# Optimization experiments

Measured on AMD Instinct MI355X. Metric: run time of the kernel, lower is better.

Reference implementation:

```python
import jax, jax.numpy as jnp
import numpy as np

NUM_HEADS = 8
DIM_HEAD = 48
SCALE = DIM_HEAD ** -0.5


def setup_inputs() -> dict:
    key = jax.random.key(0)
    k1, k2, k3 = jax.random.split(key, 3)
    B, N, D = 4, 2048, 384
    inner = NUM_HEADS * DIM_HEAD  # 384
    x = jax.random.normal(k1, (B, N, D), dtype=jnp.float32)
    # store weights in [in, out] layout (equivalent to torch Linear W.T)
    Wqkv = jax.random.normal(k2, (D, 3 * inner), dtype=jnp.float32) * (D ** -0.5)
    Wproj = jax.random.normal(k3, (inner, D), dtype=jnp.float32) * (inner ** -0.5)
    bproj = jnp.zeros((D,), dtype=jnp.float32)
    return {"x": x, "Wqkv": Wqkv, "Wproj": Wproj, "bproj": bproj}


def reference(x, Wqkv, Wproj, bproj):
    B, N, D = x.shape
    h, dh = NUM_HEADS, DIM_HEAD
    C = h * dh
    # fused QKV projection (qkv_bias=False)
    qkv = (x @ Wqkv).reshape(B, N, 3, h, dh)
    q = qkv[:, :, 0].transpose(0, 2, 1, 3)  # [B, h, N, dh]
    k = qkv[:, :, 1].transpose(0, 2, 1, 3)
    v = qkv[:, :, 2].transpose(0, 2, 1, 3)
    # naive attention: materialize [B, h, N, N] scores
    sim = jnp.einsum("bhqd,bhkd->bhqk", q, k) * SCALE
    attn = jax.nn.softmax(sim, axis=-1)
    out = jnp.einsum("bhqk,bhkd->bhqd", attn, v)  # [B, h, N, dh]
    out = out.transpose(0, 2, 1, 3).reshape(B, N, C)
    return out @ Wproj + bproj
```

## Files before the change

### kernel.cpp

```cpp
#include <hip/hip_runtime.h>
#include <hip/hip_bf16.h>


typedef _Float16 f16x8 __attribute__((ext_vector_type(8)));
typedef _Float16 f16x4 __attribute__((ext_vector_type(4)));
typedef float    f32x4 __attribute__((ext_vector_type(4)));
typedef float    f32x16 __attribute__((ext_vector_type(16)));

#define QSCL 0.20822035963448658f

__global__ __launch_bounds__(256) void prep(const float* __restrict__ wq,
                                            const float* __restrict__ wp,
                                            _Float16* __restrict__ wqt,
                                            _Float16* __restrict__ wpt)
{
    __shared__ _Float16 t[64][65];
    const int blk = blockIdx.x, tid = threadIdx.x;
    const float* src; _Float16* dst; int Nn, k0, n0;
    if (blk < 108) {
        src = wq; dst = wqt; Nn = 1152;
        k0 = (blk % 6) * 64; n0 = (blk / 6) * 64;
    } else {
        const int b2 = blk - 108;
        src = wp; dst = wpt; Nn = 384;
        k0 = (b2 % 6) * 64; n0 = (b2 / 6) * 64;
    }
    #pragma unroll
    for (int i = 0; i < 16; i++) {
        const int id = tid + i * 256;
        const int k = id >> 6, n = id & 63;
        t[k][n] = (_Float16)src[(size_t)(k0 + k) * Nn + n0 + n];
    }
    __syncthreads();
    #pragma unroll
    for (int i = 0; i < 16; i++) {
        const int id = tid + i * 256;
        const int n = id >> 6, k = id & 63;
        dst[(size_t)(n0 + n) * 384 + k0 + k] = t[k][n];
    }
}

union QkvSmem {
    struct { _Float16 As[128][72]; _Float16 Bs[64][72]; } g;
    _Float16 Ts[64][136];
    _Float16 Ts2[128][72];
};

__global__ __launch_bounds__(256) void qkv_f16(const float* __restrict__ X,
                                               const _Float16* __restrict__ Bt,
                                               _Float16* __restrict__ qh,
                                               _Float16* __restrict__ kh,
                                               _Float16* __restrict__ vt)
{
    __shared__ QkvSmem sm;
    const int tid = threadIdx.x;
    const int w = tid >> 6, lane = tid & 63, cl = lane & 15, quad = lane >> 4;
    const int bm = blockIdx.x, bn = blockIdx.y;

    f32x4 acc[2][4];
    const f32x4 z4 = {0.f, 0.f, 0.f, 0.f};
    #pragma unroll
    for (int mi = 0; mi < 2; mi++)
        #pragma unroll
        for (int t = 0; t < 4; t++) acc[mi][t] = z4;

    const int ar = tid >> 3, ac = (tid & 7) * 8;
    const float*    Ag = X  + (size_t)(bm * 128 + ar) * 384 + ac;
    const _Float16* Bg = Bt + (size_t)(bn * 64  + ar) * 384 + ac;

    float4 pa0[4], pa1[4];
    f16x8 pb[2];
    #pragma unroll
    for (int j = 0; j < 4; j++) {
        pa0[j] = *(const float4*)(Ag + (size_t)(32 * j) * 384);
        pa1[j] = *(const float4*)(Ag + (size_t)(32 * j) * 384 + 4);
    }
    #pragma unroll
    for (int j = 0; j < 2; j++) pb[j] = *(const f16x8*)(Bg + (size_t)(32 * j) * 384);

    for (int k0 = 0; k0 < 384; k0 += 64) {
        __syncthreads();
        #pragma unroll
        for (int j = 0; j < 4; j++) {
            f16x8 hh;
            hh[0] = (_Float16)pa0[j].x; hh[1] = (_Float16)pa0[j].y;
            hh[2] = (_Float16)pa0[j].z; hh[3] = (_Float16)pa0[j].w;
            hh[4] = (_Float16)pa1[j].x; hh[5] = (_Float16)pa1[j].y;
            hh[6] = (_Float16)pa1[j].z; hh[7] = (_Float16)pa1[j].w;
            *(f16x8*)&sm.g.As[ar + 32 * j][ac] = hh;
        }
        #pragma unroll
        for (int j = 0; j < 2; j++) *(f16x8*)&sm.g.Bs[ar + 32 * j][ac] = pb[j];
        __syncthreads();
        if (k0 + 64 < 384) {
            #pragma unroll
            for (int j = 0; j < 4; j++) {
                pa0[j] = *(const float4*)(Ag + (size_t)(32 * j) * 384 + k0 + 64);
                pa1[j] = *(const float4*)(Ag + (size_t)(32 * j) * 384 + k0 + 68);
            }
            #pragma unroll
            for (int j = 0; j < 2; j++)
                pb[j] = *(const f16x8*)(Bg + (size_t)(32 * j) * 384 + k0 + 64);
        }
        #pragma unroll
        for (int kh2 = 0; kh2 < 2; kh2++) {
            f16x8 bf[4];
            #pragma unroll
            for (int t = 0; t < 4; t++)
                bf[t] = *(const f16x8*)&sm.g.Bs[t * 16 + cl][kh2 * 32 + quad * 8];
            #pragma unroll
            for (int mi = 0; mi < 2; mi++) {
                const f16x8 af = *(const f16x8*)&sm.g.As[w * 32 + mi * 16 + cl][kh2 * 32 + quad * 8];
                #pragma unroll
                for (int t = 0; t < 4; t++)
                    acc[mi][t] = __builtin_amdgcn_mfma_f32_16x16x32_f16(af, bf[t], acc[mi][t], 0, 0, 0);
            }
        }
    }

    const int s = (bn * 64) / 384;
    if (s == 2) {
        __syncthreads();
        #pragma unroll
        for (int t = 0; t < 4; t++)
            #pragma unroll
            for (int mi = 0; mi < 2; mi++)
                #pragma unroll
                for (int r = 0; r < 4; r++)
                    sm.Ts[t * 16 + cl][w * 32 + mi * 16 + quad * 4 + r] =
                        (_Float16)acc[mi][t][r];
        __syncthreads();
        const int colbase = bn * 64 - 768;
        const int b  = (bm * 128) >> 11;
        const int n0 = (bm * 128) & 2047;
        #pragma unroll
        for (int i = 0; i < 4; i++) {
            const int c = i * 256 + tid;
            const int col = c >> 4, nc = c & 15;
            const int gcol = colbase + col;
            const int head = gcol / 48, d = gcol - head * 48;
            const int bh = b * 8 + head;
            *(f16x8*)&vt[(size_t)(bh * 48 + d) * 2048 + n0 + nc * 8] =
                *(const f16x8*)&sm.Ts[col][nc * 8];
        }
    } else {
        __syncthreads();
        const float scl = (s == 0) ? QSCL : 1.0f;
        #pragma unroll
        for (int t = 0; t < 4; t++)
            #pragma unroll
            for (int mi = 0; mi < 2; mi++)
                #pragma unroll
                for (int r = 0; r < 4; r++)
                    sm.Ts2[w * 32 + mi * 16 + quad * 4 + r][t * 16 + cl] =
                        (_Float16)(acc[mi][t][r] * scl);
        __syncthreads();
        _Float16* dst = (s == 0) ? qh : kh;
        const int colbase = bn * 64 - s * 384;
        const int b  = (bm * 128) >> 11;
        const int n0 = (bm * 128) & 2047;
        #pragma unroll
        for (int i = 0; i < 4; i++) {
            const int c = i * 256 + tid;
            const int row = c >> 3, ch = c & 7;
            const int gcol = colbase + ch * 8;
            const int head = gcol / 48, d = gcol - head * 48;
            const int bh = b * 8 + head;
            *(f16x8*)&dst[(size_t)(bh * 2048 + n0 + row) * 48 + d] =
                *(const f16x8*)&sm.Ts2[row][ch * 8];
        }
    }
}

union AttnSmem {
    struct {
        _Float16 Ks[64][56];
        _Float16 Vts[64][72];
    } a;
    _Float16 Ot[128][58];
};

__global__ __launch_bounds__(256) void attn_f16(const _Float16* __restrict__ qh,
                                                const _Float16* __restrict__ kh,
                                                const _Float16* __restrict__ vt,
                                                _Float16* __restrict__ ab)
{
    __shared__ AttnSmem sm;
    const int tid = threadIdx.x;
    const int w = tid >> 6, lane = tid & 63, ln = lane & 31, h = lane >> 5;
    const int bh = blockIdx.x, qt = blockIdx.y;

    for (int i = tid; i < 16 * 72; i += 256) {
        const int r = 48 + i / 72, c = i - (i / 72) * 72;
        sm.a.Vts[r][c] = (r == 48) ? (_Float16)1.0f : (_Float16)0.0f;
    }

    f16x8 qf[3];
    {
        const _Float16* qp = qh + (size_t)(bh * 2048 + qt * 128 + w * 32 + ln) * 48 + 8 * h;
        qf[0] = *(const f16x8*)qp;
        qf[1] = *(const f16x8*)(qp + 16);
        qf[2] = *(const f16x8*)(qp + 32);
    }

    f32x16 o0, o1;
    #pragma unroll
    for (int r = 0; r < 16; r++) { o0[r] = 0.f; o1[r] = 0.f; }

    const _Float16* kbase = kh + (size_t)bh * 2048 * 48;
    const _Float16* vbase = vt + (size_t)bh * 48 * 2048;

    const int kr0 = tid / 6,         kc0 = (tid % 6) * 8;
    const int kid1 = tid + 256;
    const int kr1 = kid1 / 6,        kc1 = (kid1 % 6) * 8;
    const int vr0 = tid >> 3,        vc0 = (tid & 7) * 8;
    const int vr1 = (tid + 256) >> 3;
    const int vslot_lo = 16 * ((tid & 7) >> 1) + 4 * (tid & 1);
    const _Float16* ks0 = kbase + (size_t)kr0 * 48 + kc0;
    const _Float16* ks1 = kbase + (size_t)kr1 * 48 + kc1;
    const _Float16* vs0 = vbase + (size_t)vr0 * 2048 + vc0;
    const _Float16* vs1 = vbase + (size_t)vr1 * 2048 + vc0;

    f16x8 rk0 = *(const f16x8*)ks0;
    f16x8 rv0 = *(const f16x8*)vs0;
    f16x8 rk1, rv1;
    if (tid < 128) { rk1 = *(const f16x8*)ks1; rv1 = *(const f16x8*)vs1; }

    for (int kt = 0; kt < 2048; kt += 64) {
        __syncthreads();
        *(f16x8*)&sm.a.Ks[kr0][kc0] = rk0;
        {
            const f16x4* rvh = (const f16x4*)&rv0;
            *(f16x4*)&sm.a.Vts[vr0][vslot_lo]     = rvh[0];
            *(f16x4*)&sm.a.Vts[vr0][vslot_lo + 8] = rvh[1];
        }
        if (tid < 128) {
            *(f16x8*)&sm.a.Ks[kr1][kc1] = rk1;
            const f16x4* rvh = (const f16x4*)&rv1;
            *(f16x4*)&sm.a.Vts[vr1][vslot_lo]     = rvh[0];
            *(f16x4*)&sm.a.Vts[vr1][vslot_lo + 8] = rvh[1];
        }
        __syncthreads();
        if (kt + 64 < 2048) {
            rk0 = *(const f16x8*)(ks0 + (size_t)(kt + 64) * 48);
            rv0 = *(const f16x8*)(vs0 + kt + 64);
            if (tid < 128) {
                rk1 = *(const f16x8*)(ks1 + (size_t)(kt + 64) * 48);
                rv1 = *(const f16x8*)(vs1 + kt + 64);
            }
        }

        f32x16 s0, s1;
        #pragma unroll
        for (int r = 0; r < 16; r++) { s0[r] = 0.f; s1[r] = 0.f; }
        #pragma unroll
        for (int i = 0; i < 3; i++) {
            const f16x8 ka0 = *(const f16x8*)&sm.a.Ks[ln][16 * i + 8 * h];
            s0 = __builtin_amdgcn_mfma_f32_32x32x16_f16(ka0, qf[i], s0, 0, 0, 0);
            const f16x8 ka1 = *(const f16x8*)&sm.a.Ks[32 + ln][16 * i + 8 * h];
            s1 = __builtin_amdgcn_mfma_f32_32x32x16_f16(ka1, qf[i], s1, 0, 0, 0);
        }

        f16x8 pbf[4];
        #pragma unroll
        for (int j = 0; j < 8; j++) {
            pbf[0][j] = (_Float16)exp2f(s0[j]);
            pbf[1][j] = (_Float16)exp2f(s0[8 + j]);
            pbf[2][j] = (_Float16)exp2f(s1[j]);
            pbf[3][j] = (_Float16)exp2f(s1[8 + j]);
        }

        #pragma unroll
        for (int c = 0; c < 4; c++) {
            const f16x8 av0 = *(const f16x8*)&sm.a.Vts[ln][16 * c + 8 * h];
            o0 = __builtin_amdgcn_mfma_f32_32x32x16_f16(av0, pbf[c], o0, 0, 0, 0);
            const f16x8 av1 = *(const f16x8*)&sm.a.Vts[32 + ln][16 * c + 8 * h];
            o1 = __builtin_amdgcn_mfma_f32_32x32x16_f16(av1, pbf[c], o1, 0, 0, 0);
        }
    }

    const float lr  = __shfl(o1[8], ln);
    const float inv = 1.f / lr;

    __syncthreads();
    #pragma unroll
    for (int r = 0; r < 16; r++)
        sm.Ot[w * 32 + ln][(r & 3) + 8 * (r >> 2) + 4 * h] = (_Float16)(o0[r] * inv);
    #pragma unroll
    for (int r = 0; r < 8; r++)
        sm.Ot[w * 32 + ln][32 + (r & 3) + 8 * (r >> 2) + 4 * h] = (_Float16)(o1[r] * inv);
    __syncthreads();
    const int b = bh >> 3, hd = bh & 7;
    #pragma unroll
    for (int i = 0; i < 3; i++) {
        const int c2 = i * 256 + tid;
        const int row = c2 / 6, ch = c2 % 6;
        const int q = qt * 128 + row;
        *(f16x8*)&ab[(size_t)(b * 2048 + q) * 384 + hd * 48 + ch * 8] =
            *(const f16x8*)&sm.Ot[row][ch * 8];
    }
}

__global__ __launch_bounds__(256) void proj_f16(const _Float16* __restrict__ A,
                                                const _Float16* __restrict__ Bt,
                                                const float* __restrict__ bias,
                                                float* __restrict__ out)
{
    __shared__ _Float16 As[64][72];
    __shared__ _Float16 Bs[64][72];
    const int tid = threadIdx.x;
    const int w = tid >> 6, lane = tid & 63, cl = lane & 15, quad = lane >> 4;
    const int bm = blockIdx.x, bn = blockIdx.y;

    f32x4 acc[4];
    const f32x4 z4 = {0.f, 0.f, 0.f, 0.f};
    #pragma unroll
    for (int t = 0; t < 4; t++) acc[t] = z4;

    const int ar = tid >> 3, ac = (tid & 7) * 8;
    const _Float16* Ag = A  + (size_t)(bm * 64 + ar) * 384 + ac;
    const _Float16* Bg = Bt + (size_t)(bn * 64 + ar) * 384 + ac;

    f16x8 pa[2], pb[2];
    #pragma unroll
    for (int j = 0; j < 2; j++) {
        pa[j] = *(const f16x8*)(Ag + (size_t)(32 * j) * 384);
        pb[j] = *(const f16x8*)(Bg + (size_t)(32 * j) * 384);
    }

    for (int k0 = 0; k0 < 384; k0 += 64) {
        __syncthreads();
        #pragma unroll
        for (int j = 0; j < 2; j++) {
            *(f16x8*)&As[ar + 32 * j][ac] = pa[j];
            *(f16x8*)&Bs[ar + 32 * j][ac] = pb[j];
        }
        __syncthreads();
        if (k0 + 64 < 384) {
            #pragma unroll
            for (int j = 0; j < 2; j++) {
                pa[j] = *(const f16x8*)(Ag + (size_t)(32 * j) * 384 + k0 + 64);
                pb[j] = *(const f16x8*)(Bg + (size_t)(32 * j) * 384 + k0 + 64);
            }
        }
        #pragma unroll
        for (int kh2 = 0; kh2 < 2; kh2++) {
            const f16x8 af = *(const f16x8*)&As[w * 16 + cl][kh2 * 32 + quad * 8];
            #pragma unroll
            for (int t = 0; t < 4; t++) {
                const f16x8 bf = *(const f16x8*)&Bs[t * 16 + cl][kh2 * 32 + quad * 8];
                acc[t] = __builtin_amdgcn_mfma_f32_16x16x32_f16(af, bf, acc[t], 0, 0, 0);
            }
        }
    }

    #pragma unroll
    for (int t = 0; t < 4; t++) {
        const int col = bn * 64 + t * 16 + cl;
        const float bv = bias[col];
        #pragma unroll
        for (int r = 0; r < 4; r++) {
            const int row = bm * 64 + w * 16 + quad * 4 + r;
            out[(size_t)row * 384 + col] = acc[t][r] + bv;
        }
    }
}

extern "C" void kernel_launch(void* const* d_in, const int* in_sizes, int n_in,
                              void* d_out, int out_size, void* d_ws, size_t ws_size,
                              hipStream_t stream) {
    const float* x     = (const float*)d_in[0];
    const float* Wqkv  = (const float*)d_in[1];
    const float* Wproj = (const float*)d_in[2];
    const float* bproj = (const float*)d_in[3];
    float* out = (float*)d_out;

    char* ws = (char*)d_ws;
    _Float16* wqkvt  = (_Float16*)(ws + 0);
    _Float16* wprojt = (_Float16*)(ws + 884736);
    _Float16* qh     = (_Float16*)(ws + 1179648);
    _Float16* kh     = (_Float16*)(ws + 7471104);
    _Float16* vt     = (_Float16*)(ws + 13762560);
    _Float16* ab     = (_Float16*)(ws + 20054016);

    prep<<<144, 256, 0, stream>>>(Wqkv, Wproj, wqkvt, wprojt);
    qkv_f16<<<dim3(64, 18), 256, 0, stream>>>(x, wqkvt, qh, kh, vt);
    attn_f16<<<dim3(32, 16), 256, 0, stream>>>(qh, kh, vt, ab);
    proj_f16<<<dim3(128, 6), 256, 0, stream>>>(ab, wprojt, bproj, out);
}
```

Baseline: 149.5 us.

## Pre-convert X to fp16 in prep and widen QKV GEMM tile to 128x128

The prep kernel gains extra blocks that convert the fp32 input X to fp16 in workspace. The QKV GEMM then loads fp16 A directly and uses a 128x128 output tile with a 32-wide K step instead of 128x64 with 64-wide K. This removes the per-block fp32-to-fp16 conversion that was repeated across all 18 column tiles and halves the grid's A re-reads. In exchange it adds a full write and read of an fp16 copy of X, doubles the accumulator register count, and runs more, shallower K iterations with a sync each.

```diff
diff --git a/kernel.cpp b/kernel.cpp
--- a/kernel.cpp
+++ b/kernel.cpp
@@ -9,44 +9,59 @@
 
 #define QSCL 0.20822035963448658f
 
-__global__ __launch_bounds__(256) void prep(const float* __restrict__ wq,
+__global__ __launch_bounds__(256) void prep(const float4* __restrict__ x,
+                                            const float* __restrict__ wq,
                                             const float* __restrict__ wp,
+                                            f16x4* __restrict__ xh4,
                                             _Float16* __restrict__ wqt,
                                             _Float16* __restrict__ wpt)
 {
     __shared__ _Float16 t[64][65];
     const int blk = blockIdx.x, tid = threadIdx.x;
-    const float* src; _Float16* dst; int Nn, k0, n0;
-    if (blk < 108) {
-        src = wq; dst = wqt; Nn = 1152;
-        k0 = (blk % 6) * 64; n0 = (blk / 6) * 64;
+    if (blk < 144) {
+        const float* src; _Float16* dst; int Nn, k0, n0;
+        if (blk < 108) {
+            src = wq; dst = wqt; Nn = 1152;
+            k0 = (blk % 6) * 64; n0 = (blk / 6) * 64;
+        } else {
+            const int b2 = blk - 108;
+            src = wp; dst = wpt; Nn = 384;
+            k0 = (b2 % 6) * 64; n0 = (b2 / 6) * 64;
+        }
+        #pragma unroll
+        for (int i = 0; i < 16; i++) {
+            const int id = tid + i * 256;
+            const int k = id >> 6, n = id & 63;
+            t[k][n] = (_Float16)src[(size_t)(k0 + k) * Nn + n0 + n];
+        }
+        __syncthreads();
+        #pragma unroll
+        for (int i = 0; i < 16; i++) {
+            const int id = tid + i * 256;
+            const int n = id >> 6, k = id & 63;
+            dst[(size_t)(n0 + n) * 384 + k0 + k] = t[k][n];
+        }
     } else {
-        const int b2 = blk - 108;
-        src = wp; dst = wpt; Nn = 384;
-        k0 = (b2 % 6) * 64; n0 = (b2 / 6) * 64;
-    }
-    #pragma unroll
-    for (int i = 0; i < 16; i++) {
-        const int id = tid + i * 256;
-        const int k = id >> 6, n = id & 63;
-        t[k][n] = (_Float16)src[(size_t)(k0 + k) * Nn + n0 + n];
-    }
-    __syncthreads();
-    #pragma unroll
-    for (int i = 0; i < 16; i++) {
-        const int id = tid + i * 256;
-        const int n = id >> 6, k = id & 63;
-        dst[(size_t)(n0 + n) * 384 + k0 + k] = t[k][n];
+        const int base = (blk - 144) * 3072;
+        #pragma unroll
+        for (int r = 0; r < 12; r++) {
+            const int j = base + r * 256 + tid;
+            const float4 tt = x[j];
+            f16x4 hh;
+            hh[0] = (_Float16)tt.x; hh[1] = (_Float16)tt.y;
+            hh[2] = (_Float16)tt.z; hh[3] = (_Float16)tt.w;
+            xh4[j] = hh;
+        }
     }
 }
 
 union QkvSmem {
-    struct { _Float16 As[128][72]; _Float16 Bs[64][72]; } g;
-    _Float16 Ts[64][136];
-    _Float16 Ts2[128][72];
+    struct { _Float16 As[128][40]; _Float16 Bs[128][40]; } g;
+    _Float16 Ts[128][136];
+    _Float16 Ts2[128][136];
 };
 
-__global__ __launch_bounds__(256) void qkv_f16(const float* __restrict__ X,
+__global__ __launch_bounds__(256) void qkv_f16(const _Float16* __restrict__ A,
                                                const _Float16* __restrict__ Bt,
                                                _Float16* __restrict__ qh,
                                                _Float16* __restrict__ kh,
@@ -57,72 +72,59 @@
     const int w = tid >> 6, lane = tid & 63, cl = lane & 15, quad = lane >> 4;
     const int bm = blockIdx.x, bn = blockIdx.y;
 
-    f32x4 acc[2][4];
+    f32x4 acc[2][8];
     const f32x4 z4 = {0.f, 0.f, 0.f, 0.f};
     #pragma unroll
     for (int mi = 0; mi < 2; mi++)
         #pragma unroll
-        for (int t = 0; t < 4; t++) acc[mi][t] = z4;
-
-    const int ar = tid >> 3, ac = (tid & 7) * 8;
-    const float*    Ag = X  + (size_t)(bm * 128 + ar) * 384 + ac;
-    const _Float16* Bg = Bt + (size_t)(bn * 64  + ar) * 384 + ac;
-
-    float4 pa0[4], pa1[4];
-    f16x8 pb[2];
-    #pragma unroll
-    for (int j = 0; j < 4; j++) {
-        pa0[j] = *(const float4*)(Ag + (size_t)(32 * j) * 384);
-        pa1[j] = *(const float4*)(Ag + (size_t)(32 * j) * 384 + 4);
-    }
-    #pragma unroll
-    for (int j = 0; j < 2; j++) pb[j] = *(const f16x8*)(Bg + (size_t)(32 * j) * 384);
-
-    for (int k0 = 0; k0 < 384; k0 += 64) {
-        __syncthreads();
-        #pragma unroll
-        for (int j = 0; j < 4; j++) {
-            f16x8 hh;
-            hh[0] = (_Float16)pa0[j].x; hh[1] = (_Float16)pa0[j].y;
-            hh[2] = (_Float16)pa0[j].z; hh[3] = (_Float16)pa0[j].w;
-            hh[4] = (_Float16)pa1[j].x; hh[5] = (_Float16)pa1[j].y;
-            hh[6] = (_Float16)pa1[j].z; hh[7] = (_Float16)pa1[j].w;
-            *(f16x8*)&sm.g.As[ar + 32 * j][ac] = hh;
-        }
-        #pragma unroll
-        for (int j = 0; j < 2; j++) *(f16x8*)&sm.g.Bs[ar + 32 * j][ac] = pb[j];
-        __syncthreads();
-        if (k0 + 64 < 384) {
-            #pragma unroll
-            for (int j = 0; j < 4; j++) {
-                pa0[j] = *(const float4*)(Ag + (size_t)(32 * j) * 384 + k0 + 64);
-                pa1[j] = *(const float4*)(Ag + (size_t)(32 * j) * 384 + k0 + 68);
+        for (int t = 0; t < 8; t++) acc[mi][t] = z4;
+
+    const int ar = tid >> 2, ac = (tid & 3) * 8;
+    const _Float16* Ag = A  + (size_t)(bm * 128 + ar) * 384 + ac;
+    const _Float16* Bg = Bt + (size_t)(bn * 128 + ar) * 384 + ac;
+
+    f16x8 pa[2], pb[2];
+    #pragma unroll
+    for (int j = 0; j < 2; j++) {
+        pa[j] = *(const f16x8*)(Ag + (size_t)(64 * j) * 384);
+        pb[j] = *(const f16x8*)(Bg + (size_t)(64 * j) * 384);
+    }
+
+    for (int k0 = 0; k0 < 384; k0 += 32) {
+        __syncthreads();
+        #pragma unroll
+        for (int j = 0; j < 2; j++) {
+            *(f16x8*)&sm.g.As[ar + 64 * j][ac] = pa[j];
+            *(f16x8*)&sm.g.Bs[ar + 64 * j][ac] = pb[j];
+        }
+        __syncthreads();
+        if (k0 + 32 < 384) {
+            #pragma unroll
+            for (int j = 0; j < 2; j++) {
+                pa[j] = *(const f16x8*)(Ag + (size_t)(64 * j) * 384 + k0 + 32);
+                pb[j] = *(const f16x8*)(Bg + (size_t)(64 * j) * 384 + k0 + 32);
             }
-            #pragma unroll
-            for (int j = 0; j < 2; j++)
-                pb[j] = *(const f16x8*)(Bg + (size_t)(32 * j) * 384 + k0 + 64);
-        }
-        #pragma unroll
-        for (int kh2 = 0; kh2 < 2; kh2++) {
-            f16x8 bf[4];
-            #pragma unroll
-            for (int t = 0; t < 4; t++)
-                bf[t] = *(const f16x8*)&sm.g.Bs[t * 16 + cl][kh2 * 32 + quad * 8];
-            #pragma unroll
-            for (int mi = 0; mi < 2; mi++) {
-                const f16x8 af = *(const f16x8*)&sm.g.As[w * 32 + mi * 16 + cl][kh2 * 32 + quad * 8];
-                #pragma unroll
-                for (int t = 0; t < 4; t++)
-                    acc[mi][t] = __builtin_amdgcn_mfma_f32_16x16x32_f16(af, bf[t], acc[mi][t], 0, 0, 0);
-            }
-        }
-    }
-
-    const int s = (bn * 64) / 384;
+        }
+        f16x8 bf[8];
+        #pragma unroll
+        for (int t = 0; t < 8; t++)
+            bf[t] = *(const f16x8*)&sm.g.Bs[t * 16 + cl][quad * 8];
+        #pragma unroll
+        for (int mi = 0; mi < 2; mi++) {
+            const f16x8 af = *(const f16x8*)&sm.g.As[w * 32 + mi * 16 + cl][quad * 8];
+            #pragma unroll
+            for (int t = 0; t < 8; t++)
+                acc[mi][t] = __builtin_amdgcn_mfma_f32_16x16x32_f16(af, bf[t], acc[mi][t], 0, 0, 0);
+        }
+    }
+
+    const int s = (bn * 128) / 384;
+    const int b  = (bm * 128) >> 11;
+    const int n0 = (bm * 128) & 2047;
     if (s == 2) {
         __syncthreads();
         #pragma unroll
-        for (int t = 0; t < 4; t++)
+        for (int t = 0; t < 8; t++)
             #pragma unroll
             for (int mi = 0; mi < 2; mi++)
                 #pragma unroll
@@ -130,11 +132,9 @@
                     sm.Ts[t * 16 + cl][w * 32 + mi * 16 + quad * 4 + r] =
                         (_Float16)acc[mi][t][r];
         __syncthreads();
-        const int colbase = bn * 64 - 768;
-        const int b  = (bm * 128) >> 11;
-        const int n0 = (bm * 128) & 2047;
-        #pragma unroll
-        for (int i = 0; i < 4; i++) {
+        const int colbase = bn * 128 - 768;
+        #pragma unroll
+        for (int i = 0; i < 8; i++) {
             const int c = i * 256 + tid;
             const int col = c >> 4, nc = c & 15;
             const int gcol = colbase + col;
@@ -147,7 +147,7 @@
         __syncthreads();
         const float scl = (s == 0) ? QSCL : 1.0f;
         #pragma unroll
-        for (int t = 0; t < 4; t++)
+        for (int t = 0; t < 8; t++)
             #pragma unroll
             for (int mi = 0; mi < 2; mi++)
                 #pragma unroll
@@ -156,13 +156,11 @@
                         (_Float16)(acc[mi][t][r] * scl);
         __syncthreads();
         _Float16* dst = (s == 0) ? qh : kh;
-        const int colbase = bn * 64 - s * 384;
-        const int b  = (bm * 128) >> 11;
-        const int n0 = (bm * 128) & 2047;
-        #pragma unroll
-        for (int i = 0; i < 4; i++) {
+        const int colbase = bn * 128 - s * 384;
+        #pragma unroll
+        for (int i = 0; i < 8; i++) {
             const int c = i * 256 + tid;
-            const int row = c >> 3, ch = c & 7;
+            const int row = c >> 4, ch = c & 15;
             const int gcol = colbase + ch * 8;
             const int head = gcol / 48, d = gcol - head * 48;
             const int bh = b * 8 + head;
@@ -376,15 +374,17 @@
     float* out = (float*)d_out;
 
     char* ws = (char*)d_ws;
-    _Float16* wqkvt  = (_Float16*)(ws + 0);
-    _Float16* wprojt = (_Float16*)(ws + 884736);
-    _Float16* qh     = (_Float16*)(ws + 1179648);
-    _Float16* kh     = (_Float16*)(ws + 7471104);
-    _Float16* vt     = (_Float16*)(ws + 13762560);
-    _Float16* ab     = (_Float16*)(ws + 20054016);
-
-    prep<<<144, 256, 0, stream>>>(Wqkv, Wproj, wqkvt, wprojt);
-    qkv_f16<<<dim3(64, 18), 256, 0, stream>>>(x, wqkvt, qh, kh, vt);
+    _Float16* xh     = (_Float16*)(ws + 0);
+    _Float16* wqkvt  = (_Float16*)(ws + 6291456);
+    _Float16* wprojt = (_Float16*)(ws + 7176192);
+    _Float16* qh     = (_Float16*)(ws + 7471104);
+    _Float16* kh     = (_Float16*)(ws + 13762560);
+    _Float16* vt     = (_Float16*)(ws + 20054016);
+    _Float16* ab     = (_Float16*)(ws + 26345472);
+
+    prep<<<400, 256, 0, stream>>>((const float4*)x, Wqkv, Wproj,
+                                  (f16x4*)xh, wqkvt, wprojt);
+    qkv_f16<<<dim3(64, 9), 256, 0, stream>>>(xh, wqkvt, qh, kh, vt);
     attn_f16<<<dim3(32, 16), 256, 0, stream>>>(qh, kh, vt, ab);
     proj_f16<<<dim3(128, 6), 256, 0, stream>>>(ab, wprojt, bproj, out);
 }
```

Measured after the change: 148.0 us. Within noise of the previous version (-1.0%).
